# Kernel tuning notes

Measured on AMD Instinct MI355X. Metric: run time of the kernel, lower is better.

The kernel has to match this reference:

```python
import jax, jax.numpy as jnp
import numpy as np

B, S, D = 4, 2048, 1024  # batch, seq_len, input_dim (= dk = dv)


def setup_inputs() -> dict:
    key = jax.random.key(0)
    kx, kq, kk, kv = jax.random.split(key, 4)
    scale = 1.0 / np.sqrt(D)
    return {
        "x": jax.random.normal(kx, (B, S, D), dtype=jnp.float32),
        "Wq": jax.random.normal(kq, (D, D), dtype=jnp.float32) * scale,
        "Wk": jax.random.normal(kk, (D, D), dtype=jnp.float32) * scale,
        "Wv": jax.random.normal(kv, (D, D), dtype=jnp.float32) * scale,
    }


def reference(x, Wq, Wk, Wv):
    # Linear projections (bias=False). W is [in, out].
    Q = jnp.einsum("bsd,de->bse", x, Wq)
    K = jnp.einsum("bsd,de->bse", x, Wk)
    V = jnp.einsum("bsd,de->bse", x, Wv)
    dk = Q.shape[-1]
    # scores: [B, S, S]
    scores = jnp.einsum("bqe,bke->bqk", Q, K) / jnp.sqrt(jnp.float32(dk))
    # causal mask: upper triangle (j > i) masked to -inf
    S_len = x.shape[1]
    causal = jnp.triu(jnp.ones((S_len, S_len), dtype=bool), k=1)
    scores = jnp.where(causal[None, :, :], -jnp.inf, scores)
    attn = jax.nn.softmax(scores, axis=-1)
    # dropout p=0.0 (eval): identity
    return jnp.einsum("bqk,bke->bqe", attn, V)
```

## Files before the change

### kernel.cpp

```cpp
#include <hip/hip_runtime.h>

#define S_LEN 2048
#define DMODEL 1024
#define NBATCH 4

typedef unsigned short u16;
typedef __bf16 bf16x8 __attribute__((ext_vector_type(8)));
typedef float f32x4 __attribute__((ext_vector_type(4)));

typedef __attribute__((address_space(3))) unsigned lds_u32;
typedef const __attribute__((address_space(1))) unsigned glb_u32;

__device__ __forceinline__ u16 f2bf(float f) {
  union { float f; unsigned u; } v;
  v.f = f;
  unsigned r = v.u + 0x7fffu + ((v.u >> 16) & 1u);
  return (u16)(r >> 16);
}

__device__ __forceinline__ float bf2f(u16 h) {
  union { unsigned u; float f; } v;
  v.u = ((unsigned)h) << 16;
  return v.f;
}

__global__ void convert_x_kernel(const float* __restrict__ x, u16* __restrict__ xb, long n) {
  long i = ((long)blockIdx.x * blockDim.x + threadIdx.x) * 4;
  long stride = (long)gridDim.x * blockDim.x * 4;
  for (; i < n; i += stride) {
    float4 v = *reinterpret_cast<const float4*>(x + i);
    ushort4 o;
    o.x = f2bf(v.x); o.y = f2bf(v.y); o.z = f2bf(v.z); o.w = f2bf(v.w);
    *reinterpret_cast<ushort4*>(xb + i) = o;
  }
}

__global__ void transpose_w3_kernel(const float* __restrict__ Wq, const float* __restrict__ Wk,
                                    const float* __restrict__ Wv, u16* __restrict__ Wt) {
  const float* W = blockIdx.z == 0 ? Wq : (blockIdx.z == 1 ? Wk : Wv);
  u16* dst = Wt + (long)blockIdx.z * 1024 * 1024;
  __shared__ float tile[32][33];
  int tx = threadIdx.x, ty = threadIdx.y;
  int k0 = blockIdx.x * 32, n0 = blockIdx.y * 32;
#pragma unroll
  for (int i = 0; i < 32; i += 8)
    tile[ty + i][tx] = W[(long)(k0 + ty + i) * DMODEL + n0 + tx];
  __syncthreads();
#pragma unroll
  for (int i = 0; i < 32; i += 8)
    dst[(long)(n0 + ty + i) * DMODEL + k0 + tx] = f2bf(tile[tx][ty + i]);
}

#define STG(SRCP, LD, ISB, H, T, BUFB) do { \
    const u16* _s = (SRCP) + (long)(H) * 128 * (LD) + (T) * 64; \
    char* _d = lds + (BUFB) * 65536 + ((ISB) ? 32768 : 0) + ((H) * 8 + w) * 2048; \
    __builtin_amdgcn_global_load_lds((glb_u32*)_s, (lds_u32*)_d, 16, 0, 0); \
    __builtin_amdgcn_global_load_lds((glb_u32*)(_s + 32), (lds_u32*)(_d + 1024), 16, 0, 0); \
  } while (0)

#define READ_A(QM) do { \
    _Pragma("unroll") \
    for (int _i = 0; _i < 4; ++_i) { \
      int _mp = (QM) * 8 + wm * 4 + _i; \
      af[_i][0] = *(const bf16x8*)(_Al + (_mp * 2 + 0) * 1024 + frag_off); \
      af[_i][1] = *(const bf16x8*)(_Al + (_mp * 2 + 1) * 1024 + frag_off); \
    } \
  } while (0)

#define READ_BQ(DST, QN) do { \
    _Pragma("unroll") \
    for (int _j = 0; _j < 2; ++_j) { \
      int _np = (QN) * 8 + wn * 2 + _j; \
      DST[_j][0] = *(const bf16x8*)(_Bl + (_np * 2 + 0) * 1024 + frag_off); \
      DST[_j][1] = *(const bf16x8*)(_Bl + (_np * 2 + 1) * 1024 + frag_off); \
    } \
  } while (0)

#define MFMA16(QM, QN, BREG) do { \
    _Pragma("unroll") \
    for (int _i = 0; _i < 4; ++_i) \
      _Pragma("unroll") \
      for (int _j = 0; _j < 2; ++_j) { \
        acc[QM][QN][_i][_j] = __builtin_amdgcn_mfma_f32_16x16x32_bf16(af[_i][0], BREG[_j][0], acc[QM][QN][_i][_j], 0, 0, 0); \
        acc[QM][QN][_i][_j] = __builtin_amdgcn_mfma_f32_16x16x32_bf16(af[_i][1], BREG[_j][1], acc[QM][QN][_i][_j], 0, 0, 0); \
      } \
  } while (0)

template<int CMODE, int MODE>
__global__ __launch_bounds__(512, 2) void gemm256(
    const u16* __restrict__ A, const u16* __restrict__ B,
    void* __restrict__ Cptr, void* __restrict__ Cptr2,
    int lda, int ldb, int ldc, int Kdim,
    long sAz, long sBz, long sCz)
{
  int bm = blockIdx.x, bn = blockIdx.y, bz = blockIdx.z;
  int k0 = 0, Keff = Kdim, h = 0;
  if constexpr (MODE == 1) {
    if (bn > bm) return;
  }
  if constexpr (MODE == 5) {
    h = bz & 1;
    bz >>= 1;
    int Klim = (bm + 1) * 256;
    if (h == 0) {
      Keff = Klim < 1024 ? Klim : 1024;
    } else {
      if (Klim <= 1024) return;
      k0 = 1024;
      Keff = Klim - 1024;
    }
  }
  int NT = Keff >> 6;

  const u16* Ab = A + (long)bz * sAz + (long)bm * 256 * lda + k0;
  const u16* Bb = B + (long)bz * sBz + (long)bn * 256 * ldb + k0;

  __shared__ char lds[131072];

  int tid = threadIdx.x;
  int lane = tid & 63, w = tid >> 6;
  int wm = w >> 2, wn = w & 3;
  int l15 = lane & 15, lhi = lane >> 4;
  int frag_off = (l15 * 64 + lhi * 16) ^ (((lane >> 3) & 1) << 5);

  int le = lane ^ ((lane >> 5) << 1);
  int lr = le >> 2;
  int kb = (le & 3) * 8;

  const u16* Asrc = Ab + (long)(w * 16 + lr) * lda + kb;
  const u16* Bsrc = Bb + (long)(w * 16 + lr) * ldb + kb;

  f32x4 acc[2][2][4][2];
#pragma unroll
  for (int a = 0; a < 2; ++a)
#pragma unroll
    for (int b = 0; b < 2; ++b)
#pragma unroll
      for (int c = 0; c < 4; ++c)
#pragma unroll
        for (int d = 0; d < 2; ++d)
          acc[a][b][c][d] = (f32x4){0.f, 0.f, 0.f, 0.f};

  STG(Asrc, lda, 0, 0, 0, 0); STG(Bsrc, ldb, 1, 0, 0, 0);
  STG(Asrc, lda, 0, 1, 0, 0); STG(Bsrc, ldb, 1, 1, 0, 0);
  STG(Asrc, lda, 0, 0, 1, 1); STG(Bsrc, ldb, 1, 0, 1, 1);
  asm volatile("s_waitcnt vmcnt(4)" ::: "memory");
  __builtin_amdgcn_s_barrier();

  for (int g = 0; g < NT; ++g) {
    int buf = g & 1;
    int t1 = g + 1; if (t1 >= NT) t1 -= NT;
    int t2 = g + 2; if (t2 >= NT) t2 -= NT;
    const char* _Al = lds + buf * 65536;
    const char* _Bl = _Al + 32768;
    bf16x8 af[4][2], b0[2][2], b1[2][2];

    READ_A(0);
    READ_BQ(b0, 0);
    STG(Asrc, lda, 0, 1, t1, buf ^ 1);
    __builtin_amdgcn_s_barrier();
    asm volatile("s_waitcnt lgkmcnt(0)" ::: "memory");
    __builtin_amdgcn_sched_barrier(0);
    __builtin_amdgcn_s_setprio(1);
    MFMA16(0, 0, b0);
    __builtin_amdgcn_s_setprio(0);
    __builtin_amdgcn_s_barrier();

    READ_BQ(b1, 1);
    STG(Bsrc, ldb, 1, 1, t1, buf ^ 1);
    __builtin_amdgcn_s_barrier();
    asm volatile("s_waitcnt lgkmcnt(0)" ::: "memory");
    __builtin_amdgcn_sched_barrier(0);
    __builtin_amdgcn_s_setprio(1);
    MFMA16(0, 1, b1);
    __builtin_amdgcn_s_setprio(0);
    __builtin_amdgcn_s_barrier();

    READ_A(1);
    STG(Asrc, lda, 0, 0, t2, buf);
    __builtin_amdgcn_s_barrier();
    asm volatile("s_waitcnt lgkmcnt(0)" ::: "memory");
    __builtin_amdgcn_sched_barrier(0);
    __builtin_amdgcn_s_setprio(1);
    MFMA16(1, 1, b1);
    __builtin_amdgcn_s_setprio(0);
    __builtin_amdgcn_s_barrier();

    STG(Bsrc, ldb, 1, 0, t2, buf);
    __builtin_amdgcn_s_barrier();
    __builtin_amdgcn_s_setprio(1);
    MFMA16(1, 0, b0);
    __builtin_amdgcn_s_setprio(0);
    asm volatile("s_waitcnt vmcnt(4)" ::: "memory");
    __builtin_amdgcn_s_barrier();
  }

  int Mbase = bm * 256, Nbase = bn * 256;
#pragma unroll
  for (int qm = 0; qm < 2; ++qm)
#pragma unroll
    for (int qn = 0; qn < 2; ++qn)
#pragma unroll
      for (int i = 0; i < 4; ++i)
#pragma unroll
        for (int j = 0; j < 2; ++j) {
          int rl = qm * 128 + wm * 64 + i * 16 + lhi * 4;
          int col = Nbase + qn * 128 + wn * 32 + j * 16 + l15;
          f32x4 v = acc[qm][qn][i][j];
          if constexpr (CMODE == 1) {
            u16* C = (u16*)Cptr + (long)bz * sCz;
            int r0 = Mbase + rl;
#pragma unroll
            for (int r = 0; r < 4; ++r)
              C[(long)(r0 + r) * ldc + col] = f2bf(v[r]);
          } else {
            if (h == 0) {
              float* O = (float*)Cptr2 + (long)bz * S_LEN * 1024;
              int row = Mbase + rl;
#pragma unroll
              for (int r = 0; r < 4; ++r)
                O[(long)(row + r) * 1024 + col] = v[r];
            } else {
              float* Pp = (float*)Cptr + ((long)(bz * 1024 + (bm - 4) * 256 + rl)) * 1024 + col;
#pragma unroll
              for (int r = 0; r < 4; ++r)
                Pp[(long)r * 1024] = v[r];
            }
          }
        }
}

__global__ __launch_bounds__(512) void gemm_proj(
    const u16* __restrict__ A, const u16* __restrict__ B, void* __restrict__ Cptr,
    int lda, int ldb, int Kdim)
{
  int bm = blockIdx.x, bn = blockIdx.y;
  int NT = Kdim >> 5;

  const u16* Ab = A + (long)bm * 128 * lda;
  const u16* Bb = B + (long)bn * 256 * ldb;

  __shared__ char lds[73728];

  int tid = threadIdx.x;
  int lane = tid & 63, w = tid >> 6;
  int wm = w >> 2, wn = w & 3;
  int l15 = lane & 15, lhi = lane >> 4;
  int frag_off = (l15 * 64 + lhi * 16) ^ (((lane >> 3) & 1) << 5);

  int le = lane ^ ((lane >> 5) << 1);
  int lr = le >> 2;
  int kb = (le & 3) * 8;

  const u16* Asrc = Ab + (long)(w * 16 + lr) * lda + kb;
  const u16* Bsrc = Bb + (long)(w * 16 + lr) * ldb + kb;

#define STG32(T, BI) do { \
    const u16* _sa = Asrc + (T) * 32; \
    const u16* _sb = Bsrc + (T) * 32; \
    char* _base = lds + (BI) * 24576; \
    __builtin_amdgcn_global_load_lds((glb_u32*)_sa, (lds_u32*)(_base + w * 1024), 16, 0, 0); \
    __builtin_amdgcn_global_load_lds((glb_u32*)_sb, (lds_u32*)(_base + 8192 + w * 1024), 16, 0, 0); \
    __builtin_amdgcn_global_load_lds((glb_u32*)(_sb + (long)128 * ldb), (lds_u32*)(_base + 8192 + (8 + w) * 1024), 16, 0, 0); \
  } while (0)

  f32x4 acc[4][4];
#pragma unroll
  for (int i = 0; i < 4; ++i)
#pragma unroll
    for (int j = 0; j < 4; ++j)
      acc[i][j] = (f32x4){0.f, 0.f, 0.f, 0.f};

  STG32(0, 0);
  STG32(1, 1);
  asm volatile("s_waitcnt vmcnt(3)" ::: "memory");
  __builtin_amdgcn_s_barrier();

  int buf = 0;
  for (int g = 0; g < NT; ++g) {
    bool issue = (g + 2 < NT);
    if (issue) {
      int b2 = buf + 2; if (b2 >= 3) b2 -= 3;
      STG32(g + 2, b2);
    }

    const char* _Al = lds + buf * 24576;
    const char* _Bl = _Al + 8192;
    bf16x8 af[4], bf[4];
#pragma unroll
    for (int i = 0; i < 4; ++i)
      af[i] = *(const bf16x8*)(_Al + (wm * 4 + i) * 1024 + frag_off);
#pragma unroll
    for (int j = 0; j < 4; ++j)
      bf[j] = *(const bf16x8*)(_Bl + (wn * 4 + j) * 1024 + frag_off);

    asm volatile("s_waitcnt lgkmcnt(0)" ::: "memory");
    __builtin_amdgcn_sched_barrier(0);
    __builtin_amdgcn_s_setprio(1);
#pragma unroll
    for (int i = 0; i < 4; ++i)
#pragma unroll
      for (int j = 0; j < 4; ++j)
        acc[i][j] = __builtin_amdgcn_mfma_f32_16x16x32_bf16(af[i], bf[j], acc[i][j], 0, 0, 0);
    __builtin_amdgcn_s_setprio(0);

    if (issue) {
      asm volatile("s_waitcnt vmcnt(3)" ::: "memory");
    } else {
      asm volatile("s_waitcnt vmcnt(0)" ::: "memory");
    }
    __builtin_amdgcn_s_barrier();

    ++buf; if (buf >= 3) buf = 0;
  }
#undef STG32

#pragma unroll
  for (int i = 0; i < 4; ++i)
#pragma unroll
    for (int j = 0; j < 4; ++j) {
      int rl = wm * 64 + i * 16 + lhi * 4;
      int col = bn * 256 + wn * 64 + j * 16 + l15;
      f32x4 v = acc[i][j];
      int r0 = bm * 128 + rl;
      if (col < 2048) {
        u16* dst = (u16*)Cptr + (col >= 1024 ? 8388608 : 0);
        int c = col & 1023;
#pragma unroll
        for (int r = 0; r < 4; ++r)
          dst[(long)(r0 + r) * 1024 + c] = f2bf(v[r]);
      } else {
        u16* Vt = (u16*)Cptr + 16777216;
        int e = col - 2048;
        int bb = r0 >> 11, s = r0 & 2047;
        ushort4 u;
        u.x = f2bf(v[0]); u.y = f2bf(v[1]); u.z = f2bf(v[2]); u.w = f2bf(v[3]);
        *reinterpret_cast<ushort4*>(Vt + ((long)bb * 1024 + e) * 2048 + s) = u;
      }
    }
}

__global__ __launch_bounds__(256) void softmax1p(const u16* __restrict__ sc,
                                                 u16* __restrict__ P) {
  int q = blockIdx.x, b = blockIdx.y;
  const u16* srow = sc + ((long)b * S_LEN + q) * S_LEN;
  u16* prow = P + ((long)b * S_LEN + q) * S_LEN;
  int n = q + 1;
  int nz = ((q >> 8) + 1) << 8;
  int tid = threadIdx.x;
  int j0 = tid * 8;
  const float scale = 0.03125f;

  __shared__ float red[8];

  float vs[8];
#pragma unroll
  for (int e = 0; e < 8; ++e) vs[e] = -1e30f;
  if (j0 < n) {
    ushort4 a = *reinterpret_cast<const ushort4*>(srow + j0);
    ushort4 c = *reinterpret_cast<const ushort4*>(srow + j0 + 4);
    vs[0] = bf2f(a.x) * scale; vs[1] = bf2f(a.y) * scale;
    vs[2] = bf2f(a.z) * scale; vs[3] = bf2f(a.w) * scale;
    vs[4] = bf2f(c.x) * scale; vs[5] = bf2f(c.y) * scale;
    vs[6] = bf2f(c.z) * scale; vs[7] = bf2f(c.w) * scale;
#pragma unroll
    for (int e = 0; e < 8; ++e)
      if (j0 + e >= n) vs[e] = -1e30f;
  }

  float m = -1e30f;
#pragma unroll
  for (int e = 0; e < 8; ++e) m = fmaxf(m, vs[e]);
#pragma unroll
  for (int off = 32; off > 0; off >>= 1) m = fmaxf(m, __shfl_xor(m, off, 64));
  if ((tid & 63) == 0) red[tid >> 6] = m;
  __syncthreads();
  float ms = fmaxf(fmaxf(red[0], red[1]), fmaxf(red[2], red[3]));

  float p[8];
  float s = 0.f;
#pragma unroll
  for (int e = 0; e < 8; ++e) { p[e] = __expf(vs[e] - ms); s += (j0 + e < n) ? p[e] : 0.f; }
#pragma unroll
  for (int off = 32; off > 0; off >>= 1) s += __shfl_xor(s, off, 64);
  __syncthreads();
  if ((tid & 63) == 0) red[4 + (tid >> 6)] = s;
  __syncthreads();
  float inv = 1.f / (red[4] + red[5] + red[6] + red[7]);

  if (j0 < nz) {
    ushort4 o0, o1;
    o0.x = (j0 + 0 < n) ? f2bf(p[0] * inv) : (u16)0;
    o0.y = (j0 + 1 < n) ? f2bf(p[1] * inv) : (u16)0;
    o0.z = (j0 + 2 < n) ? f2bf(p[2] * inv) : (u16)0;
    o0.w = (j0 + 3 < n) ? f2bf(p[3] * inv) : (u16)0;
    o1.x = (j0 + 4 < n) ? f2bf(p[4] * inv) : (u16)0;
    o1.y = (j0 + 5 < n) ? f2bf(p[5] * inv) : (u16)0;
    o1.z = (j0 + 6 < n) ? f2bf(p[6] * inv) : (u16)0;
    o1.w = (j0 + 7 < n) ? f2bf(p[7] * inv) : (u16)0;
    *reinterpret_cast<ushort4*>(prow + j0) = o0;
    *reinterpret_cast<ushort4*>(prow + j0 + 4) = o1;
  }
}

__global__ __launch_bounds__(256) void add_pv(const float4* __restrict__ p2,
                                              float4* __restrict__ out) {
  long i = (long)blockIdx.x * 256 + threadIdx.x;
  int c4 = (int)(i & 255);
  long rp = i >> 8;
  int b = (int)(rp >> 10), r = (int)(rp & 1023);
  long oo = ((long)(b * 2048 + 1024 + r) << 8) + c4;
  float4 a = out[oo], d = p2[i];
  a.x += d.x; a.y += d.y; a.z += d.z; a.w += d.w;
  out[oo] = a;
}

extern "C" void kernel_launch(void* const* d_in, const int* in_sizes, int n_in,
                              void* d_out, int out_size, void* d_ws, size_t ws_size,
                              hipStream_t stream) {
  const float* x  = (const float*)d_in[0];
  const float* Wq = (const float*)d_in[1];
  const float* Wk = (const float*)d_in[2];
  const float* Wv = (const float*)d_in[3];
  float* out = (float*)d_out;

  char* ws = (char*)d_ws;
  u16*   xb    = (u16*)(ws);
  u16*   wtb   = (u16*)(ws + 16777216);
  u16*   Qb    = (u16*)(ws + 23068672);
  u16*   Kb    = (u16*)(ws + 39845888);
  u16*   Vtb   = (u16*)(ws + 56623104);
  u16*   scb   = (u16*)(ws + 73400320);
  float* part2 = (float*)(ws + 73400320);
  u16*   P     = (u16*)(ws + 115343360);

  long nx = (long)NBATCH * S_LEN * DMODEL;
  convert_x_kernel<<<2048, 256, 0, stream>>>(x, xb, nx);

  transpose_w3_kernel<<<dim3(32, 32, 3), dim3(32, 8), 0, stream>>>(Wq, Wk, Wv, wtb);

  gemm_proj<<<dim3(64, 12, 1), 512, 0, stream>>>(xb, wtb, Qb, DMODEL, DMODEL, DMODEL);

  gemm256<1, 1><<<dim3(8, 8, 4), 512, 0, stream>>>(
      Qb, Kb, scb, nullptr, DMODEL, DMODEL, S_LEN, DMODEL,
      (long)S_LEN * DMODEL, (long)S_LEN * DMODEL, (long)S_LEN * S_LEN);

  softmax1p<<<dim3(S_LEN, NBATCH), 256, 0, stream>>>(scb, P);

  gemm256<6, 5><<<dim3(8, 4, 8), 512, 0, stream>>>(
      P, Vtb, part2, out, S_LEN, S_LEN, 0, S_LEN,
      (long)S_LEN * S_LEN, (long)DMODEL * S_LEN, 0);

  add_pv<<<4096, 256, 0, stream>>>((const float4*)part2, (float4*)out);
}
```

Before: 170.7 us.

## Replace 256x256 BK64 attention GEMMs with 128x256 BK32 triple-buffered kernel

Replaces the 256x256 tile, BK=64, double-buffered GEMM used for QK^T and PV with a 128x256 tile, BK=32 kernel that keeps three LDS stages and a simpler single-phase MFMA loop. The smaller M tile makes the causal skipping finer (128-row granularity), so fewer masked scores are computed and the softmax zero-fill boundary drops to 128. This cuts wasted causal work and LDS footprint. In exchange there is less data reuse per tile, more blocks, and the more elaborate interleaved prefetch schedule is lost.

Result: no change. 168.9 us (-1.0%).

```diff
diff --git a/kernel.cpp b/kernel.cpp
--- a/kernel.cpp
+++ b/kernel.cpp
@@ -51,43 +51,8 @@
     dst[(long)(n0 + ty + i) * DMODEL + k0 + tx] = f2bf(tile[tx][ty + i]);
 }
 
-#define STG(SRCP, LD, ISB, H, T, BUFB) do { \
-    const u16* _s = (SRCP) + (long)(H) * 128 * (LD) + (T) * 64; \
-    char* _d = lds + (BUFB) * 65536 + ((ISB) ? 32768 : 0) + ((H) * 8 + w) * 2048; \
-    __builtin_amdgcn_global_load_lds((glb_u32*)_s, (lds_u32*)_d, 16, 0, 0); \
-    __builtin_amdgcn_global_load_lds((glb_u32*)(_s + 32), (lds_u32*)(_d + 1024), 16, 0, 0); \
-  } while (0)
-
-#define READ_A(QM) do { \
-    _Pragma("unroll") \
-    for (int _i = 0; _i < 4; ++_i) { \
-      int _mp = (QM) * 8 + wm * 4 + _i; \
-      af[_i][0] = *(const bf16x8*)(_Al + (_mp * 2 + 0) * 1024 + frag_off); \
-      af[_i][1] = *(const bf16x8*)(_Al + (_mp * 2 + 1) * 1024 + frag_off); \
-    } \
-  } while (0)
-
-#define READ_BQ(DST, QN) do { \
-    _Pragma("unroll") \
-    for (int _j = 0; _j < 2; ++_j) { \
-      int _np = (QN) * 8 + wn * 2 + _j; \
-      DST[_j][0] = *(const bf16x8*)(_Bl + (_np * 2 + 0) * 1024 + frag_off); \
-      DST[_j][1] = *(const bf16x8*)(_Bl + (_np * 2 + 1) * 1024 + frag_off); \
-    } \
-  } while (0)
-
-#define MFMA16(QM, QN, BREG) do { \
-    _Pragma("unroll") \
-    for (int _i = 0; _i < 4; ++_i) \
-      _Pragma("unroll") \
-      for (int _j = 0; _j < 2; ++_j) { \
-        acc[QM][QN][_i][_j] = __builtin_amdgcn_mfma_f32_16x16x32_bf16(af[_i][0], BREG[_j][0], acc[QM][QN][_i][_j], 0, 0, 0); \
-        acc[QM][QN][_i][_j] = __builtin_amdgcn_mfma_f32_16x16x32_bf16(af[_i][1], BREG[_j][1], acc[QM][QN][_i][_j], 0, 0, 0); \
-      } \
-  } while (0)
-
 template<int CMODE, int MODE>
-__global__ __launch_bounds__(512, 2) void gemm256(
+__global__ __launch_bounds__(512) void gemm_bk32(
     const u16* __restrict__ A, const u16* __restrict__ B,
     void* __restrict__ Cptr, void* __restrict__ Cptr2,
     int lda, int ldb, int ldc, int Kdim,
@@ -96,26 +61,23 @@
   int bm = blockIdx.x, bn = blockIdx.y, bz = blockIdx.z;
   int k0 = 0, Keff = Kdim, h = 0;
   if constexpr (MODE == 1) {
-    if (bn > bm) return;
-  }
-  if constexpr (MODE == 5) {
+    if (bn * 2 > bm) return;
+  }
+  if constexpr (MODE == 4) {
     h = bz & 1;
     bz >>= 1;
-    int Klim = (bm + 1) * 256;
-    if (h == 0) {
-      Keff = Klim < 1024 ? Klim : 1024;
-    } else {
-      if (Klim <= 1024) return;
-      k0 = 1024;
-      Keff = Klim - 1024;
-    }
-  }
-  int NT = Keff >> 6;
-
-  const u16* Ab = A + (long)bz * sAz + (long)bm * 256 * lda + k0;
+    int Klim = (bm + 1) * 128;
+    k0 = h * 1024;
+    if (k0 >= Klim) return;
+    int k1 = k0 + 1024; if (k1 > Klim) k1 = Klim;
+    Keff = k1 - k0;
+  }
+  int NT = Keff >> 5;
+
+  const u16* Ab = A + (long)bz * sAz + (long)bm * 128 * lda + k0;
   const u16* Bb = B + (long)bz * sBz + (long)bn * 256 * ldb + k0;
 
-  __shared__ char lds[131072];
+  __shared__ char lds[73728];
 
   int tid = threadIdx.x;
   int lane = tid & 63, w = tid >> 6;
@@ -130,104 +92,94 @@
   const u16* Asrc = Ab + (long)(w * 16 + lr) * lda + kb;
   const u16* Bsrc = Bb + (long)(w * 16 + lr) * ldb + kb;
 
-  f32x4 acc[2][2][4][2];
-#pragma unroll
-  for (int a = 0; a < 2; ++a)
-#pragma unroll
-    for (int b = 0; b < 2; ++b)
-#pragma unroll
-      for (int c = 0; c < 4; ++c)
-#pragma unroll
-        for (int d = 0; d < 2; ++d)
-          acc[a][b][c][d] = (f32x4){0.f, 0.f, 0.f, 0.f};
-
-  STG(Asrc, lda, 0, 0, 0, 0); STG(Bsrc, ldb, 1, 0, 0, 0);
-  STG(Asrc, lda, 0, 1, 0, 0); STG(Bsrc, ldb, 1, 1, 0, 0);
-  STG(Asrc, lda, 0, 0, 1, 1); STG(Bsrc, ldb, 1, 0, 1, 1);
-  asm volatile("s_waitcnt vmcnt(4)" ::: "memory");
+#define STG32(T, BI) do { \
+    const u16* _sa = Asrc + (T) * 32; \
+    const u16* _sb = Bsrc + (T) * 32; \
+    char* _base = lds + (BI) * 24576; \
+    __builtin_amdgcn_global_load_lds((glb_u32*)_sa, (lds_u32*)(_base + w * 1024), 16, 0, 0); \
+    __builtin_amdgcn_global_load_lds((glb_u32*)_sb, (lds_u32*)(_base + 8192 + w * 1024), 16, 0, 0); \
+    __builtin_amdgcn_global_load_lds((glb_u32*)(_sb + (long)128 * ldb), (lds_u32*)(_base + 8192 + (8 + w) * 1024), 16, 0, 0); \
+  } while (0)
+
+  f32x4 acc[4][4];
+#pragma unroll
+  for (int i = 0; i < 4; ++i)
+#pragma unroll
+    for (int j = 0; j < 4; ++j)
+      acc[i][j] = (f32x4){0.f, 0.f, 0.f, 0.f};
+
+  STG32(0, 0);
+  STG32(1, 1);
+  asm volatile("s_waitcnt vmcnt(3)" ::: "memory");
   __builtin_amdgcn_s_barrier();
 
+  int buf = 0;
   for (int g = 0; g < NT; ++g) {
-    int buf = g & 1;
-    int t1 = g + 1; if (t1 >= NT) t1 -= NT;
-    int t2 = g + 2; if (t2 >= NT) t2 -= NT;
-    const char* _Al = lds + buf * 65536;
-    const char* _Bl = _Al + 32768;
-    bf16x8 af[4][2], b0[2][2], b1[2][2];
-
-    READ_A(0);
-    READ_BQ(b0, 0);
-    STG(Asrc, lda, 0, 1, t1, buf ^ 1);
-    __builtin_amdgcn_s_barrier();
+    bool issue = (g + 2 < NT);
+    if (issue) {
+      int b2 = buf + 2; if (b2 >= 3) b2 -= 3;
+      STG32(g + 2, b2);
+    }
+
+    const char* _Al = lds + buf * 24576;
+    const char* _Bl = _Al + 8192;
+    bf16x8 af[4], bf[4];
+#pragma unroll
+    for (int i = 0; i < 4; ++i)
+      af[i] = *(const bf16x8*)(_Al + (wm * 4 + i) * 1024 + frag_off);
+#pragma unroll
+    for (int j = 0; j < 4; ++j)
+      bf[j] = *(const bf16x8*)(_Bl + (wn * 4 + j) * 1024 + frag_off);
+
     asm volatile("s_waitcnt lgkmcnt(0)" ::: "memory");
     __builtin_amdgcn_sched_barrier(0);
     __builtin_amdgcn_s_setprio(1);
-    MFMA16(0, 0, b0);
+#pragma unroll
+    for (int i = 0; i < 4; ++i)
+#pragma unroll
+      for (int j = 0; j < 4; ++j)
+        acc[i][j] = __builtin_amdgcn_mfma_f32_16x16x32_bf16(af[i], bf[j], acc[i][j], 0, 0, 0);
     __builtin_amdgcn_s_setprio(0);
+
+    if (issue) {
+      asm volatile("s_waitcnt vmcnt(3)" ::: "memory");
+    } else {
+      asm volatile("s_waitcnt vmcnt(0)" ::: "memory");
+    }
     __builtin_amdgcn_s_barrier();
 
-    READ_BQ(b1, 1);
-    STG(Bsrc, ldb, 1, 1, t1, buf ^ 1);
-    __builtin_amdgcn_s_barrier();
-    asm volatile("s_waitcnt lgkmcnt(0)" ::: "memory");
-    __builtin_amdgcn_sched_barrier(0);
-    __builtin_amdgcn_s_setprio(1);
-    MFMA16(0, 1, b1);
-    __builtin_amdgcn_s_setprio(0);
-    __builtin_amdgcn_s_barrier();
-
-    READ_A(1);
-    STG(Asrc, lda, 0, 0, t2, buf);
-    __builtin_amdgcn_s_barrier();
-    asm volatile("s_waitcnt lgkmcnt(0)" ::: "memory");
-    __builtin_amdgcn_sched_barrier(0);
-    __builtin_amdgcn_s_setprio(1);
-    MFMA16(1, 1, b1);
-    __builtin_amdgcn_s_setprio(0);
-    __builtin_amdgcn_s_barrier();
-
-    STG(Bsrc, ldb, 1, 0, t2, buf);
-    __builtin_amdgcn_s_barrier();
-    __builtin_amdgcn_s_setprio(1);
-    MFMA16(1, 0, b0);
-    __builtin_amdgcn_s_setprio(0);
-    asm volatile("s_waitcnt vmcnt(4)" ::: "memory");
-    __builtin_amdgcn_s_barrier();
-  }
-
-  int Mbase = bm * 256, Nbase = bn * 256;
-#pragma unroll
-  for (int qm = 0; qm < 2; ++qm)
-#pragma unroll
-    for (int qn = 0; qn < 2; ++qn)
-#pragma unroll
-      for (int i = 0; i < 4; ++i)
-#pragma unroll
-        for (int j = 0; j < 2; ++j) {
-          int rl = qm * 128 + wm * 64 + i * 16 + lhi * 4;
-          int col = Nbase + qn * 128 + wn * 32 + j * 16 + l15;
-          f32x4 v = acc[qm][qn][i][j];
-          if constexpr (CMODE == 1) {
-            u16* C = (u16*)Cptr + (long)bz * sCz;
-            int r0 = Mbase + rl;
-#pragma unroll
-            for (int r = 0; r < 4; ++r)
-              C[(long)(r0 + r) * ldc + col] = f2bf(v[r]);
-          } else {
-            if (h == 0) {
-              float* O = (float*)Cptr2 + (long)bz * S_LEN * 1024;
-              int row = Mbase + rl;
-#pragma unroll
-              for (int r = 0; r < 4; ++r)
-                O[(long)(row + r) * 1024 + col] = v[r];
-            } else {
-              float* Pp = (float*)Cptr + ((long)(bz * 1024 + (bm - 4) * 256 + rl)) * 1024 + col;
-#pragma unroll
-              for (int r = 0; r < 4; ++r)
-                Pp[(long)r * 1024] = v[r];
-            }
-          }
+    ++buf; if (buf >= 3) buf = 0;
+  }
+#undef STG32
+
+#pragma unroll
+  for (int i = 0; i < 4; ++i)
+#pragma unroll
+    for (int j = 0; j < 4; ++j) {
+      int rl = wm * 64 + i * 16 + lhi * 4;
+      int col = bn * 256 + wn * 64 + j * 16 + l15;
+      f32x4 v = acc[i][j];
+      if constexpr (CMODE == 1) {
+        u16* C = (u16*)Cptr + (long)bz * sCz;
+        int r0 = bm * 128 + rl;
+#pragma unroll
+        for (int r = 0; r < 4; ++r)
+          C[(long)(r0 + r) * ldc + col] = f2bf(v[r]);
+      } else {
+        if (h == 0) {
+          float* O = (float*)Cptr2 + (long)bz * S_LEN * 1024;
+          int row = bm * 128 + rl;
+#pragma unroll
+          for (int r = 0; r < 4; ++r)
+            O[(long)(row + r) * 1024 + col] = v[r];
+        } else {
+          float* Pp = (float*)Cptr + ((long)((bz * 8 + bm - 8) * 128 + rl)) * 1024 + col;
+#pragma unroll
+          for (int r = 0; r < 4; ++r)
+            Pp[(long)r * 1024] = v[r];
         }
+      }
+    }
 }
 
 __global__ __launch_bounds__(512) void gemm_proj(
@@ -346,7 +298,7 @@
   const u16* srow = sc + ((long)b * S_LEN + q) * S_LEN;
   u16* prow = P + ((long)b * S_LEN + q) * S_LEN;
   int n = q + 1;
-  int nz = ((q >> 8) + 1) << 8;
+  int nz = ((q >> 7) + 1) << 7;
   int tid = threadIdx.x;
   int j0 = tid * 8;
   const float scale = 0.03125f;
@@ -441,13 +393,13 @@
 
   gemm_proj<<<dim3(64, 12, 1), 512, 0, stream>>>(xb, wtb, Qb, DMODEL, DMODEL, DMODEL);
 
-  gemm256<1, 1><<<dim3(8, 8, 4), 512, 0, stream>>>(
+  gemm_bk32<1, 1><<<dim3(16, 8, 4), 512, 0, stream>>>(
       Qb, Kb, scb, nullptr, DMODEL, DMODEL, S_LEN, DMODEL,
       (long)S_LEN * DMODEL, (long)S_LEN * DMODEL, (long)S_LEN * S_LEN);
 
   softmax1p<<<dim3(S_LEN, NBATCH), 256, 0, stream>>>(scb, P);
 
-  gemm256<6, 5><<<dim3(8, 4, 8), 512, 0, stream>>>(
+  gemm_bk32<5, 4><<<dim3(16, 4, 8), 512, 0, stream>>>(
       P, Vtb, part2, out, S_LEN, S_LEN, 0, S_LEN,
       (long)S_LEN * S_LEN, (long)DMODEL * S_LEN, 0);
 
```
